# Optimization experiments

Measured on AMD Instinct MI355X. Metric: run time of the kernel, lower is better.

## Reference

```python
import jax, jax.numpy as jnp
import numpy as np

B, T, F = 1024, 256, 124
H = 64
ADIM = 4


def setup_inputs() -> dict:
    key = jax.random.key(0)
    ks = jax.random.split(key, 8)
    s = 0.05
    return {
        "x": jax.random.normal(ks[0], (B, T, F), dtype=jnp.float32),
        "previous_actions": jax.random.normal(ks[1], (B, T, ADIM), dtype=jnp.float32),
        "Wx": jax.random.normal(ks[2], (F + ADIM, 4 * H), dtype=jnp.float32) * s,
        "Wh": jax.random.normal(ks[3], (H, 4 * H), dtype=jnp.float32) * s,
        "b": jnp.zeros((4 * H,), dtype=jnp.float32),
        "W1": jax.random.normal(ks[4], (T * H, 64), dtype=jnp.float32) * s,
        "b1": jnp.zeros((64,), dtype=jnp.float32),
        "W2": jax.random.normal(ks[5], (64, 64), dtype=jnp.float32) * s,
        "b2": jnp.zeros((64,), dtype=jnp.float32),
        "W3": jax.random.normal(ks[6], (64, 2 * ADIM), dtype=jnp.float32) * s,
        "b3": jnp.zeros((2 * ADIM,), dtype=jnp.float32),
    }


def _lstm_scan(xs, Wx, Wh, b):
    # xs: [B, T, D]; returns final (c, h) and all hidden states [B, T, H]
    bsz = xs.shape[0]
    h_dim = Wh.shape[0]
    # precompute input projections once (big GEMM), scan only does h @ Wh
    xproj = jnp.einsum('btd,dg->btg', xs, Wx) + b  # [B, T, 4H]

    def step(carry, xp):
        c, h = carry
        gates = xp + h @ Wh  # [B, 4H]
        i, f, g, o = jnp.split(gates, 4, axis=-1)
        i = jax.nn.sigmoid(i)
        f = jax.nn.sigmoid(f)
        g = jnp.tanh(g)
        o = jax.nn.sigmoid(o)
        c = f * c + i * g
        h = o * jnp.tanh(c)
        return (c, h), h

    c0 = jnp.zeros((bsz, h_dim), xs.dtype)
    h0 = jnp.zeros((bsz, h_dim), xs.dtype)
    (c, h), hs = jax.lax.scan(step, (c0, h0), jnp.swapaxes(xproj, 0, 1))
    return (c, h), jnp.swapaxes(hs, 0, 1)  # hs: [B, T, H]


def reference(x, previous_actions, Wx, Wh, b, W1, b1, W2, b2, W3, b3):
    bsz, seq = x.shape[0], x.shape[1]
    xf = x.reshape((bsz, seq, -1))
    xs = jnp.concatenate([xf, previous_actions], axis=-1)  # [B, T, F+4]
    (c, h), hs = _lstm_scan(xs, Wx, Wh, b)
    flat = hs.reshape((bsz, -1))  # [B, T*H] -- module flattens ALL timesteps
    a = jax.nn.relu(flat @ W1 + b1)
    a = jax.nn.relu(a @ W2 + b2)
    actor = a @ W3 + b3  # [B, 2*action_dim]
    return actor, (c, h)
```

## Files before the change

kernel.cpp:

```cpp
#include <hip/hip_runtime.h>
#include <hip/hip_bf16.h>
#include <stdint.h>

static constexpr int Bsz = 1024;
static constexpr int TT  = 256;
static constexpr int FF  = 124;
static constexpr int HH  = 64;
static constexpr int GG  = 256;
static constexpr int BB  = 16;
static constexpr int C_OFF = Bsz * 8;
static constexpr int H_OFF = C_OFF + Bsz * HH;

static constexpr int WXH_U16 = 24 * 256 * 8;
static constexpr int W1P_U16 = 256 * 4096;
static constexpr size_t WS_NEED = (size_t)(WXH_U16 + W1P_U16) * 2;

static constexpr int XS0 = 0;
static constexpr int XP0 = 65536;
static constexpr int HB0 = 131072;
static constexpr int MA0 = 135168;
static constexpr int MB0 = 139328;
static constexpr int POOLSZ = 143488;

typedef __attribute__((ext_vector_type(8))) short bf16x8;
typedef __attribute__((ext_vector_type(4))) float f32x4;

#define MFMA16 __builtin_amdgcn_mfma_f32_16x16x32_bf16

__device__ __forceinline__ uint16_t f2bf(float x) {
  union { float f; uint32_t u; } v; v.f = x;
  return (uint16_t)((v.u + 0x7FFFu + ((v.u >> 16) & 1u)) >> 16);
}
__device__ __forceinline__ uint32_t cvtpk(float lo, float hi) {
  uint32_t r;
  asm("v_cvt_pk_bf16_f32 %0, %1, %2" : "=v"(r) : "v"(lo), "v"(hi));
  return r;
}
__device__ __forceinline__ uint16_t bf1(float x) { return (uint16_t)cvtpk(x, x); }
__device__ __forceinline__ float fsig(float x) {
  return __builtin_amdgcn_rcpf(1.0f + __builtin_amdgcn_exp2f(-1.4426950408889634f * x));
}
__device__ __forceinline__ float ftanh(float x) {
  float e = __builtin_amdgcn_exp2f(-2.8853900817779268f * x);
  return (1.0f - e) * __builtin_amdgcn_rcpf(1.0f + e);
}
__device__ __forceinline__ bf16x8 cvt8(float4 a, float4 b) {
  union { uint32_t u[4]; bf16x8 v; } r;
  r.u[0] = cvtpk(a.x, a.y); r.u[1] = cvtpk(a.z, a.w);
  r.u[2] = cvtpk(b.x, b.y); r.u[3] = cvtpk(b.z, b.w);
  return r.v;
}
__device__ __forceinline__ void dma16(const void* g, void* l) {
  __builtin_amdgcn_global_load_lds(
      (const __attribute__((address_space(1))) uint32_t*)g,
      (__attribute__((address_space(3))) uint32_t*)l, 16, 0, 0);
}

__global__ __launch_bounds__(256) void pack_weights(
    const float* __restrict__ Wx, const float* __restrict__ Wh,
    const float* __restrict__ W1, uint16_t* __restrict__ wsp)
{
  const int c = blockIdx.x * 256 + threadIdx.x;
  uint16_t v[8];
  size_t dst;
  if (c < 6144) {
    const int f = c >> 8, tid = c & 255;
    const int w = tid >> 6, l = tid & 63;
    const int kgl = (l >> 4) * 8, r16 = l & 15;
    if (f < 16) {
      const int g = f >> 2, kf = f & 3;
      const int col = g * 64 + w * 16 + r16;
#pragma unroll
      for (int j = 0; j < 8; ++j) v[j] = f2bf(Wx[(size_t)(kf * 32 + kgl + j) * GG + col]);
    } else {
      const int g = (f - 16) >> 1, kf = (f - 16) & 1;
      const int col = g * 64 + w * 16 + r16;
#pragma unroll
      for (int j = 0; j < 8; ++j) v[j] = f2bf(Wh[(size_t)(kf * 32 + kgl + j) * GG + col]);
    }
    dst = (size_t)c * 8;
  } else if (c < 6144 + 131072) {
    const int cc = c - 6144;
    const int t = cc >> 9, r = cc & 511;
    const int w = r >> 7, half = (r >> 6) & 1, l = r & 63;
    const int row0 = t * 64 + half * 32 + (l >> 4) * 8;
    const int col = w * 16 + (l & 15);
#pragma unroll
    for (int j = 0; j < 8; ++j) v[j] = f2bf(W1[(size_t)(row0 + j) * 64 + col]);
    dst = (size_t)WXH_U16 + (size_t)cc * 8;
  } else return;
  uint4 pk;
  pk.x = (uint32_t)v[0] | ((uint32_t)v[1] << 16);
  pk.y = (uint32_t)v[2] | ((uint32_t)v[3] << 16);
  pk.z = (uint32_t)v[4] | ((uint32_t)v[5] << 16);
  pk.w = (uint32_t)v[6] | ((uint32_t)v[7] << 16);
  *(uint4*)(wsp + dst) = pk;
}


#define PER_PROD(PRT, U) { \
  asm volatile("s_waitcnt vmcnt(6)" ::: "memory"); \
  const bool live_ = (PRT) + 2 < TT; \
  bf16x8 ax0, ax1, ax2, ax3; \
  if (live_) { \
    const char* xb = pool + (((U) + 2) & 7) * 8192; \
    float4 y0 = *(const float4*)(xb + offx0); \
    float4 y1 = *(const float4*)(xb + offx1); \
    float4 y2 = *(const float4*)(xb + offx2); \
    float4 y3 = *(const float4*)(xb + offx3); \
    ax0 = cvt8(y0, y1); ax1 = cvt8(y2, y3); \
    float4 y4 = *(const float4*)(xb + offx4); \
    float4 y5 = *(const float4*)(xb + offx5); \
    float4 y6 = *(const float4*)(xb + offx6); \
    float4 y7 = *(const float4*)(xb + offx7); \
    ax2 = cvt8(y4, y5); ax3 = cvt8(y6, y7); \
  } \
  { char* ld = pool + (((U) + 6) & 7) * 8192 + pw * 2048; \
    dma16(gsrc0, ld); dma16(gsrc1, ld + 1024); } \
  if ((PRT) + 7 < TT) { gsrc0 += inc0; gsrc1 += inc1; } \
  if (live_) { \
    char* xpw = pool + XP0 + (((U) + 2) & 3) * 16384 + pw * 4096 + l * 16; \
    _Pragma("unroll") \
    for (int g = 0; g < 4; ++g) { \
      f32x4 acc = {bias4[g], bias4[g], bias4[g], bias4[g]}; \
      acc = MFMA16(ax0, bwx[g][0], acc, 0, 0, 0); \
      acc = MFMA16(ax1, bwx[g][1], acc, 0, 0, 0); \
      acc = MFMA16(ax2, bwx[g][2], acc, 0, 0, 0); \
      acc = MFMA16(ax3, bwx[g][3], acc, 0, 0, 0); \
      *(f32x4*)(xpw + g * 1024) = acc; \
    } \
  } }

#define PER_CONS(PRT, U) { \
  const uint16_t* w1p = wsp + (size_t)WXH_U16 + ((size_t)(PRT) * 512 + cs * 128 + l) * 8; \
  bf16x8 nw1a = *(const bf16x8*)(w1p); \
  bf16x8 nw1b = *(const bf16x8*)(w1p + 512); \
  const char* xpb = pool + XP0 + ((U) & 3) * 16384 + cs * 4096 + l * 16; \
  f32x4 a0 = *(const f32x4*)(xpb); \
  f32x4 a1 = *(const f32x4*)(xpb + 1024); \
  f32x4 a2 = *(const f32x4*)(xpb + 2048); \
  f32x4 a3 = *(const f32x4*)(xpb + 3072); \
  const char* hb = pool + HB0 + ((U) & 1) * 2048; \
  bf16x8 ah0 = *(const bf16x8*)(hb + row16 * 128 + (((0 + kg) << 4) ^ swz)); \
  bf16x8 ah1 = *(const bf16x8*)(hb + row16 * 128 + (((4 + kg) << 4) ^ swz)); \
  a0 = MFMA16(ah0, bwh[0][0], a0, 0, 0, 0); \
  a1 = MFMA16(ah0, bwh[1][0], a1, 0, 0, 0); \
  a2 = MFMA16(ah0, bwh[2][0], a2, 0, 0, 0); \
  a3 = MFMA16(ah0, bwh[3][0], a3, 0, 0, 0); \
  a0 = MFMA16(ah1, bwh[0][1], a0, 0, 0, 0); \
  a1 = MFMA16(ah1, bwh[1][1], a1, 0, 0, 0); \
  a2 = MFMA16(ah1, bwh[2][1], a2, 0, 0, 0); \
  a3 = MFMA16(ah1, bwh[3][1], a3, 0, 0, 0); \
  wacc = MFMA16(ah0, cw1a, wacc, 0, 0, 0); \
  wacc = MFMA16(ah1, cw1b, wacc, 0, 0, 0); \
  cw1a = nw1a; cw1b = nw1b; \
  char* hw = pool + HB0 + (((U) & 1) ^ 1) * 2048; \
  _Pragma("unroll") \
  for (int jj = 0; jj < 4; ++jj) { \
    float i_ = fsig(a0[jj]); \
    float f_ = fsig(a1[jj]); \
    float gv = ftanh(a2[jj]); \
    float o_ = fsig(a3[jj]); \
    float cn = f_ * cacc[jj] + i_ * gv; \
    cacc[jj] = cn; \
    float hv = o_ * ftanh(cn); \
    const int row = kg * 4 + jj; \
    *(uint16_t*)(hw + row * 128 + (((kcol >> 3) << 4) ^ ((row & 7) << 4)) + (kcol & 7) * 2) = bf1(hv); \
  } }

#define PERIOD(PRT, U) { \
  if (w < 4) { PER_CONS(PRT, U) } else { PER_PROD(PRT, U) } \
  asm volatile("s_waitcnt lgkmcnt(0)\n\ts_barrier" ::: "memory"); }

__global__ __launch_bounds__(512, 2)
void actor_pc(
    const float* __restrict__ x,  const float* __restrict__ pa,
    const float* __restrict__ bg, const uint16_t* __restrict__ wsp,
    const float* __restrict__ b1, const float* __restrict__ W2,
    const float* __restrict__ b2, const float* __restrict__ W3,
    const float* __restrict__ b3, float* __restrict__ out)
{
  __shared__ __align__(16) char pool[POOLSZ];

  const int tid   = threadIdx.x;
  const int w     = tid >> 6;
  const int cs    = w & 3;
  const int pw    = w & 3;
  const int l     = tid & 63;
  const int row16 = l & 15;
  const int kg    = l >> 4;
  const int b0    = blockIdx.x * BB;
  const int swz   = (row16 & 7) << 4;
  const int kcol  = cs * 16 + row16;

  if (w < 4) __builtin_amdgcn_s_setprio(1);

  bf16x8 bwx[4][4];
  bf16x8 bwh[4][2];
  float  bias4[4];
  bf16x8 cw1a = {}, cw1b = {};
  float  cacc[4] = {0.f, 0.f, 0.f, 0.f};
  f32x4  wacc = {0.f, 0.f, 0.f, 0.f};

  int offx0, offx1, offx2, offx3, offx4, offx5, offx6, offx7;
  {
    const int rb = row16 * 512, r7 = row16 & 7;
#define OX(kf, lh) (rb + ((((kf) * 8 + kg * 2 + (lh)) ^ r7) << 4))
    offx0 = OX(0, 0); offx1 = OX(0, 1); offx2 = OX(1, 0); offx3 = OX(1, 1);
    offx4 = OX(2, 0); offx5 = OX(2, 1); offx6 = OX(3, 0); offx7 = OX(3, 1);
#undef OX
  }
  const char* gsrc0; const char* gsrc1; int inc0 = 0, inc1 = 0;
  {
#define GSRC(j, G, INC) { \
    const int d = pw * 2 + (j); \
    const int row = d * 2 + (l >> 5); \
    const int c_swz = l & 31; \
    const int c_or = c_swz ^ (row & 7); \
    const size_t rb_ = (size_t)(b0 + row) * TT; \
    if (c_or == 31) { G = (const char*)(pa + rb_ * 4); INC = 16; } \
    else { G = (const char*)(x + rb_ * FF + c_or * 4); INC = FF * 4; } }
    GSRC(0, gsrc0, inc0)
    GSRC(1, gsrc1, inc1)
#undef GSRC
  }

  if (w >= 4) {
#pragma unroll
    for (int g = 0; g < 4; ++g) {
#pragma unroll
      for (int kf = 0; kf < 4; ++kf)
        bwx[g][kf] = *(const bf16x8*)(wsp + ((size_t)(g * 4 + kf) * 256 + pw * 64 + l) * 8);
      bias4[g] = bg[g * 64 + pw * 16 + row16];
    }
#pragma unroll
    for (int s = 0; s < 6; ++s) {
      char* ld = pool + s * 8192 + pw * 2048;
      dma16(gsrc0, ld); dma16(gsrc1, ld + 1024);
      gsrc0 += inc0; gsrc1 += inc1;
    }
  } else {
#pragma unroll
    for (int g = 0; g < 4; ++g)
#pragma unroll
      for (int kf = 0; kf < 2; ++kf)
        bwh[g][kf] = *(const bf16x8*)(wsp + ((size_t)(16 + g * 2 + kf) * 256 + cs * 64 + l) * 8);
    const uint16_t* w1p = wsp + (size_t)WXH_U16 + ((size_t)cs * 128 + l) * 8;
    cw1a = *(const bf16x8*)(w1p);
    cw1b = *(const bf16x8*)(w1p + 512);
  }
  if (tid < 256) ((uint64_t*)(pool + HB0))[tid] = 0ull;

#define PRE(TSTEP, VMC) \
  if (w >= 4) { \
    asm volatile("s_waitcnt vmcnt(" #VMC ")" ::: "memory"); \
    const char* xb = pool + (TSTEP) * 8192; \
    float4 y0 = *(const float4*)(xb + offx0), y1 = *(const float4*)(xb + offx1); \
    float4 y2 = *(const float4*)(xb + offx2), y3 = *(const float4*)(xb + offx3); \
    float4 y4 = *(const float4*)(xb + offx4), y5 = *(const float4*)(xb + offx5); \
    float4 y6 = *(const float4*)(xb + offx6), y7 = *(const float4*)(xb + offx7); \
    bf16x8 ax0 = cvt8(y0, y1), ax1 = cvt8(y2, y3), ax2 = cvt8(y4, y5), ax3 = cvt8(y6, y7); \
    char* xpw = pool + XP0 + (TSTEP) * 16384 + pw * 4096 + l * 16; \
    _Pragma("unroll") \
    for (int g = 0; g < 4; ++g) { \
      f32x4 acc = {bias4[g], bias4[g], bias4[g], bias4[g]}; \
      acc = MFMA16(ax0, bwx[g][0], acc, 0, 0, 0); \
      acc = MFMA16(ax1, bwx[g][1], acc, 0, 0, 0); \
      acc = MFMA16(ax2, bwx[g][2], acc, 0, 0, 0); \
      acc = MFMA16(ax3, bwx[g][3], acc, 0, 0, 0); \
      *(f32x4*)(xpw + g * 1024) = acc; \
    } \
  } \
  asm volatile("s_waitcnt lgkmcnt(0)\n\ts_barrier" ::: "memory");

  PRE(0, 10)
  PRE(1, 8)
#undef PRE

#pragma unroll 1
  for (int pp = 0; pp < TT; pp += 8) {
    PERIOD(pp + 0, 0) PERIOD(pp + 1, 1) PERIOD(pp + 2, 2) PERIOD(pp + 3, 3)
    PERIOD(pp + 4, 4) PERIOD(pp + 5, 5) PERIOD(pp + 6, 6) PERIOD(pp + 7, 7)
  }

  __syncthreads();

  {
    float* w2l = (float*)pool;
    for (int i = tid; i < 4096; i += 512) w2l[i] = W2[i];
  }

  if (w < 4) {
    const char* hb = pool + HB0;
    bf16x8 at0 = *(const bf16x8*)(hb + row16 * 128 + (((0 + kg) << 4) ^ swz));
    bf16x8 at1 = *(const bf16x8*)(hb + row16 * 128 + (((4 + kg) << 4) ^ swz));
    wacc = MFMA16(at0, cw1a, wacc, 0, 0, 0);
    wacc = MFMA16(at1, cw1b, wacc, 0, 0, 0);
    const float bv = b1[kcol];
    float* mlpa = (float*)(pool + MA0);
#pragma unroll
    for (int jj = 0; jj < 4; ++jj) {
      const int row = kg * 4 + jj;
      mlpa[row * 65 + kcol] = fmaxf(wacc[jj] + bv, 0.f);
      out[C_OFF + (size_t)(b0 + row) * HH + kcol] = cacc[jj];
      uint32_t hu = *(const uint16_t*)(hb + row * 128 +
                    (((kcol >> 3) << 4) ^ ((row & 7) << 4)) + (kcol & 7) * 2);
      union { uint32_t u; float f; } hf_; hf_.u = hu << 16;
      out[H_OFF + (size_t)(b0 + row) * HH + kcol] = hf_.f;
    }
  }
  __syncthreads();
  {
    const float* mlpa = (const float*)(pool + MA0);
    const float* w2l  = (const float*)pool;
    float* mlpb = (float*)(pool + MB0);
    const int b = tid >> 5, j0 = tid & 31;
    float s0 = b2[j0], s1 = b2[j0 + 32];
#pragma unroll 8
    for (int k = 0; k < 64; ++k) {
      const float av = mlpa[b * 65 + k];
      s0 += av * w2l[k * 64 + j0];
      s1 += av * w2l[k * 64 + j0 + 32];
    }
    mlpb[b * 65 + j0]      = fmaxf(s0, 0.f);
    mlpb[b * 65 + j0 + 32] = fmaxf(s1, 0.f);
  }
  __syncthreads();
  if (tid < 128) {
    const float* mlpb = (const float*)(pool + MB0);
    const int b = tid >> 3, jj = tid & 7;
    float s = b3[jj];
#pragma unroll 8
    for (int k = 0; k < 64; ++k) s += mlpb[b * 65 + k] * W3[(size_t)k * 8 + jj];
    out[(size_t)(b0 + b) * 8 + jj] = s;
  }
}

__global__ __launch_bounds__(256, 1) void actor_fused_fb(
    const float* __restrict__ x,  const float* __restrict__ pa,
    const float* __restrict__ Wx, const float* __restrict__ Wh,
    const float* __restrict__ bg, const float* __restrict__ W1,
    const float* __restrict__ b1, const float* __restrict__ W2,
    const float* __restrict__ b2, const float* __restrict__ W3,
    const float* __restrict__ b3, float* __restrict__ out)
{
  __shared__ __align__(16) uint16_t xs_lds[2][BB * 128];
  __shared__ __align__(16) uint16_t h_lds[2][BB * HH];
  __shared__ float w2_lds[64 * 64];
  __shared__ float mlp_a[BB * 65];
  __shared__ float mlp_b[BB * 65];

  const int tid = threadIdx.x, w = tid >> 6, l = tid & 63;
  const int row16 = l & 15, kg = l >> 4;
  const int b0 = blockIdx.x * BB, swz = (row16 & 7) << 4;

  bf16x8 bwx[4][4], bwh[4][2];
  float bias4[4];
#pragma unroll
  for (int g = 0; g < 4; ++g) {
    const int col = g * 64 + w * 16 + row16;
    bias4[g] = bg[col];
#pragma unroll
    for (int kf = 0; kf < 4; ++kf)
#pragma unroll
      for (int j = 0; j < 8; ++j)
        bwx[g][kf][j] = (short)f2bf(Wx[(size_t)(kf * 32 + kg * 8 + j) * GG + col]);
#pragma unroll
    for (int kf = 0; kf < 2; ++kf)
#pragma unroll
      for (int j = 0; j < 8; ++j)
        bwh[g][kf][j] = (short)f2bf(Wh[(size_t)(kf * 32 + kg * 8 + j) * GG + col]);
  }
  for (int i = tid; i < 64 * 64; i += 256) w2_lds[i] = W2[i];
  reinterpret_cast<uint64_t*>(&h_lds[0][0])[tid] = 0ull;

  const int srow = tid >> 4, li = tid & 15;
  const int st_byte = srow * 256 + ((li << 4) ^ ((srow & 7) << 4));
  {
    const size_t base = (size_t)(b0 + srow) * TT + 0;
    float4 fa, fb;
    if (li < 15) { fa = *(const float4*)(x + base * FF + li * 8);
                   fb = *(const float4*)(x + base * FF + li * 8 + 4); }
    else         { fa = *(const float4*)(x + base * FF + 120);
                   fb = *(const float4*)(pa + base * 4); }
    uint4 pk;
    pk.x = (uint32_t)f2bf(fa.x) | ((uint32_t)f2bf(fa.y) << 16);
    pk.y = (uint32_t)f2bf(fa.z) | ((uint32_t)f2bf(fa.w) << 16);
    pk.z = (uint32_t)f2bf(fb.x) | ((uint32_t)f2bf(fb.y) << 16);
    pk.w = (uint32_t)f2bf(fb.z) | ((uint32_t)f2bf(fb.w) << 16);
    *(uint4*)((char*)&xs_lds[0][0] + st_byte) = pk;
  }
  float4 pfa, pfb;
  {
    const size_t base = (size_t)(b0 + srow) * TT + 1;
    if (li < 15) { pfa = *(const float4*)(x + base * FF + li * 8);
                   pfb = *(const float4*)(x + base * FF + li * 8 + 4); }
    else         { pfa = *(const float4*)(x + base * FF + 120);
                   pfb = *(const float4*)(pa + base * 4); }
  }
  __syncthreads();

  f32x4 cacc = {0.f, 0.f, 0.f, 0.f};
  f32x4 wacc = {0.f, 0.f, 0.f, 0.f};
  int cur = 0;

  for (int t = 0; t < TT; ++t) {
    {
      uint4 pk;
      pk.x = (uint32_t)f2bf(pfa.x) | ((uint32_t)f2bf(pfa.y) << 16);
      pk.y = (uint32_t)f2bf(pfa.z) | ((uint32_t)f2bf(pfa.w) << 16);
      pk.z = (uint32_t)f2bf(pfb.x) | ((uint32_t)f2bf(pfb.y) << 16);
      pk.w = (uint32_t)f2bf(pfb.z) | ((uint32_t)f2bf(pfb.w) << 16);
      *(uint4*)((char*)&xs_lds[cur ^ 1][0] + st_byte) = pk;
    }
    {
      const int tp = (t + 2 < TT) ? (t + 2) : (TT - 1);
      const size_t base = (size_t)(b0 + srow) * TT + tp;
      if (li < 15) { pfa = *(const float4*)(x + base * FF + li * 8);
                     pfb = *(const float4*)(x + base * FF + li * 8 + 4); }
      else         { pfa = *(const float4*)(x + base * FF + 120);
                     pfb = *(const float4*)(pa + base * 4); }
    }
    bf16x8 bw1a, bw1b;
    if (t > 0) {
      const size_t r0 = (size_t)(t - 1) * 64 + kg * 8;
      const int c1w = w * 16 + row16;
#pragma unroll
      for (int j = 0; j < 8; ++j) {
        bw1a[j] = (short)f2bf(W1[(r0 + j) * 64 + c1w]);
        bw1b[j] = (short)f2bf(W1[(r0 + 32 + j) * 64 + c1w]);
      }
    }
    const char* xb = (const char*)&xs_lds[cur][0];
    const char* hb = (const char*)&h_lds[cur][0];
    bf16x8 ax0 = *(const bf16x8*)(xb + row16 * 256 + (((0 * 4 + kg) << 4) ^ swz));
    bf16x8 ax1 = *(const bf16x8*)(xb + row16 * 256 + (((1 * 4 + kg) << 4) ^ swz));
    bf16x8 ax2 = *(const bf16x8*)(xb + row16 * 256 + (((2 * 4 + kg) << 4) ^ swz));
    bf16x8 ax3 = *(const bf16x8*)(xb + row16 * 256 + (((3 * 4 + kg) << 4) ^ swz));
    bf16x8 ah0 = *(const bf16x8*)(hb + row16 * 128 + (((0 + kg) << 4) ^ swz));
    bf16x8 ah1 = *(const bf16x8*)(hb + row16 * 128 + (((4 + kg) << 4) ^ swz));

    f32x4 g0 = {bias4[0], bias4[0], bias4[0], bias4[0]};
    f32x4 g1 = {bias4[1], bias4[1], bias4[1], bias4[1]};
    f32x4 g2 = {bias4[2], bias4[2], bias4[2], bias4[2]};
    f32x4 g3 = {bias4[3], bias4[3], bias4[3], bias4[3]};
    g0 = MFMA16(ax0, bwx[0][0], g0, 0, 0, 0);
    g1 = MFMA16(ax0, bwx[1][0], g1, 0, 0, 0);
    g2 = MFMA16(ax0, bwx[2][0], g2, 0, 0, 0);
    g3 = MFMA16(ax0, bwx[3][0], g3, 0, 0, 0);
    g0 = MFMA16(ax1, bwx[0][1], g0, 0, 0, 0);
    g1 = MFMA16(ax1, bwx[1][1], g1, 0, 0, 0);
    g2 = MFMA16(ax1, bwx[2][1], g2, 0, 0, 0);
    g3 = MFMA16(ax1, bwx[3][1], g3, 0, 0, 0);
    g0 = MFMA16(ax2, bwx[0][2], g0, 0, 0, 0);
    g1 = MFMA16(ax2, bwx[1][2], g1, 0, 0, 0);
    g2 = MFMA16(ax2, bwx[2][2], g2, 0, 0, 0);
    g3 = MFMA16(ax2, bwx[3][2], g3, 0, 0, 0);
    g0 = MFMA16(ax3, bwx[0][3], g0, 0, 0, 0);
    g1 = MFMA16(ax3, bwx[1][3], g1, 0, 0, 0);
    g2 = MFMA16(ax3, bwx[2][3], g2, 0, 0, 0);
    g3 = MFMA16(ax3, bwx[3][3], g3, 0, 0, 0);
    g0 = MFMA16(ah0, bwh[0][0], g0, 0, 0, 0);
    g1 = MFMA16(ah0, bwh[1][0], g1, 0, 0, 0);
    g2 = MFMA16(ah0, bwh[2][0], g2, 0, 0, 0);
    g3 = MFMA16(ah0, bwh[3][0], g3, 0, 0, 0);
    g0 = MFMA16(ah1, bwh[0][1], g0, 0, 0, 0);
    g1 = MFMA16(ah1, bwh[1][1], g1, 0, 0, 0);
    g2 = MFMA16(ah1, bwh[2][1], g2, 0, 0, 0);
    g3 = MFMA16(ah1, bwh[3][1], g3, 0, 0, 0);
    if (t > 0) {
      wacc = MFMA16(ah0, bw1a, wacc, 0, 0, 0);
      wacc = MFMA16(ah1, bw1b, wacc, 0, 0, 0);
    }
    const int kcol = w * 16 + row16;
#pragma unroll
    for (int jj = 0; jj < 4; ++jj) {
      float i_ = fsig(g0[jj]);
      float f_ = fsig(g1[jj]);
      float gv = ftanh(g2[jj]);
      float o_ = fsig(g3[jj]);
      float cn = f_ * cacc[jj] + i_ * gv;
      cacc[jj] = cn;
      float hv = o_ * ftanh(cn);
      const int row = kg * 4 + jj;
      *(uint16_t*)((char*)&h_lds[cur ^ 1][0] + row * 128 +
                   (((kcol >> 3) << 4) ^ ((row & 7) << 4)) + (kcol & 7) * 2) = f2bf(hv);
      if (t == TT - 1) {
        out[C_OFF + (size_t)(b0 + row) * HH + kcol] = cn;
        out[H_OFF + (size_t)(b0 + row) * HH + kcol] = hv;
      }
    }
    __syncthreads();
    cur ^= 1;
  }
  {
    const char* hb = (const char*)&h_lds[cur][0];
    bf16x8 at0 = *(const bf16x8*)(hb + row16 * 128 + (((0 + kg) << 4) ^ swz));
    bf16x8 at1 = *(const bf16x8*)(hb + row16 * 128 + (((4 + kg) << 4) ^ swz));
    bf16x8 bw1a, bw1b;
    const size_t r0 = (size_t)(TT - 1) * 64 + kg * 8;
    const int c1w = w * 16 + row16;
#pragma unroll
    for (int j = 0; j < 8; ++j) {
      bw1a[j] = (short)f2bf(W1[(r0 + j) * 64 + c1w]);
      bw1b[j] = (short)f2bf(W1[(r0 + 32 + j) * 64 + c1w]);
    }
    wacc = MFMA16(at0, bw1a, wacc, 0, 0, 0);
    wacc = MFMA16(at1, bw1b, wacc, 0, 0, 0);
  }
  {
    const int kcol = w * 16 + row16;
    const float bv = b1[kcol];
#pragma unroll
    for (int jj = 0; jj < 4; ++jj)
      mlp_a[(kg * 4 + jj) * 65 + kcol] = fmaxf(wacc[jj] + bv, 0.f);
  }
  __syncthreads();
  {
    const int b = tid >> 4, j0 = tid & 15;
    float s0 = b2[j0], s1 = b2[j0 + 16], s2 = b2[j0 + 32], s3 = b2[j0 + 48];
#pragma unroll 8
    for (int k = 0; k < 64; ++k) {
      const float av = mlp_a[b * 65 + k];
      s0 += av * w2_lds[k * 64 + j0];
      s1 += av * w2_lds[k * 64 + j0 + 16];
      s2 += av * w2_lds[k * 64 + j0 + 32];
      s3 += av * w2_lds[k * 64 + j0 + 48];
    }
    mlp_b[b * 65 + j0]      = fmaxf(s0, 0.f);
    mlp_b[b * 65 + j0 + 16] = fmaxf(s1, 0.f);
    mlp_b[b * 65 + j0 + 32] = fmaxf(s2, 0.f);
    mlp_b[b * 65 + j0 + 48] = fmaxf(s3, 0.f);
  }
  __syncthreads();
  if (tid < 128) {
    const int b = tid >> 3, jj = tid & 7;
    float s = b3[jj];
#pragma unroll 8
    for (int k = 0; k < 64; ++k) s += mlp_b[b * 65 + k] * W3[(size_t)k * 8 + jj];
    out[(size_t)(b0 + b) * 8 + jj] = s;
  }
}

extern "C" void kernel_launch(void* const* d_in, const int* in_sizes, int n_in,
                              void* d_out, int out_size, void* d_ws, size_t ws_size,
                              hipStream_t stream) {
  const float* x  = (const float*)d_in[0];
  const float* pa = (const float*)d_in[1];
  const float* Wx = (const float*)d_in[2];
  const float* Wh = (const float*)d_in[3];
  const float* bg = (const float*)d_in[4];
  const float* W1 = (const float*)d_in[5];
  const float* b1 = (const float*)d_in[6];
  const float* W2 = (const float*)d_in[7];
  const float* b2 = (const float*)d_in[8];
  const float* W3 = (const float*)d_in[9];
  const float* b3 = (const float*)d_in[10];
  (void)in_sizes; (void)n_in; (void)out_size;

  if (ws_size >= WS_NEED) {
    uint16_t* wsp = (uint16_t*)d_ws;
    pack_weights<<<dim3(536), dim3(256), 0, stream>>>(Wx, Wh, W1, wsp);
    actor_pc<<<dim3(Bsz / BB), dim3(512), 0, stream>>>(
        x, pa, bg, wsp, b1, W2, b2, W3, b3, (float*)d_out);
  } else {
    actor_fused_fb<<<dim3(Bsz / BB), dim3(256), 0, stream>>>(
        x, pa, Wx, Wh, bg, W1, b1, W2, b2, W3, b3, (float*)d_out);
  }
}
```

Before: 189.3 us.

## Merge producer/consumer warps into single 4-wave block with register-held input projections

Replaces the 8-wave producer/consumer warp-specialized LSTM kernel with a 4-wave kernel where every wave computes the next step's input projection itself and keeps it in registers (double-buffered XPA/XPB), eliminating the LDS round-trip for xproj. W1 tiles are now streamed into an LDS ring via async DMA instead of per-step global loads. This shrinks LDS use and halves threads, trading inter-wave overlap for lower LDS traffic and register pressure on the serial recurrence path.

New measurement: 210.0 us. 1.11x slower.

```diff
diff --git a/kernel.cpp b/kernel.cpp
--- a/kernel.cpp
+++ b/kernel.cpp
@@ -15,12 +15,12 @@
 static constexpr int W1P_U16 = 256 * 4096;
 static constexpr size_t WS_NEED = (size_t)(WXH_U16 + W1P_U16) * 2;
 
-static constexpr int XS0 = 0;
-static constexpr int XP0 = 65536;
-static constexpr int HB0 = 131072;
-static constexpr int MA0 = 135168;
-static constexpr int MB0 = 139328;
-static constexpr int POOLSZ = 143488;
+static constexpr int XS0  = 0;
+static constexpr int W1R0 = 65536;
+static constexpr int HB0  = 98304;
+static constexpr int MA0  = 102400;
+static constexpr int MB0  = 106560;
+static constexpr int POOLSZ = 110720;
 
 typedef __attribute__((ext_vector_type(8))) short bf16x8;
 typedef __attribute__((ext_vector_type(4))) float f32x4;
@@ -97,52 +97,15 @@
   *(uint4*)(wsp + dst) = pk;
 }
 
-
-#define PER_PROD(PRT, U) { \
-  asm volatile("s_waitcnt vmcnt(6)" ::: "memory"); \
-  const bool live_ = (PRT) + 2 < TT; \
-  bf16x8 ax0, ax1, ax2, ax3; \
-  if (live_) { \
-    const char* xb = pool + (((U) + 2) & 7) * 8192; \
-    float4 y0 = *(const float4*)(xb + offx0); \
-    float4 y1 = *(const float4*)(xb + offx1); \
-    float4 y2 = *(const float4*)(xb + offx2); \
-    float4 y3 = *(const float4*)(xb + offx3); \
-    ax0 = cvt8(y0, y1); ax1 = cvt8(y2, y3); \
-    float4 y4 = *(const float4*)(xb + offx4); \
-    float4 y5 = *(const float4*)(xb + offx5); \
-    float4 y6 = *(const float4*)(xb + offx6); \
-    float4 y7 = *(const float4*)(xb + offx7); \
-    ax2 = cvt8(y4, y5); ax3 = cvt8(y6, y7); \
-  } \
-  { char* ld = pool + (((U) + 6) & 7) * 8192 + pw * 2048; \
-    dma16(gsrc0, ld); dma16(gsrc1, ld + 1024); } \
-  if ((PRT) + 7 < TT) { gsrc0 += inc0; gsrc1 += inc1; } \
-  if (live_) { \
-    char* xpw = pool + XP0 + (((U) + 2) & 3) * 16384 + pw * 4096 + l * 16; \
-    _Pragma("unroll") \
-    for (int g = 0; g < 4; ++g) { \
-      f32x4 acc = {bias4[g], bias4[g], bias4[g], bias4[g]}; \
-      acc = MFMA16(ax0, bwx[g][0], acc, 0, 0, 0); \
-      acc = MFMA16(ax1, bwx[g][1], acc, 0, 0, 0); \
-      acc = MFMA16(ax2, bwx[g][2], acc, 0, 0, 0); \
-      acc = MFMA16(ax3, bwx[g][3], acc, 0, 0, 0); \
-      *(f32x4*)(xpw + g * 1024) = acc; \
-    } \
-  } }
-
-#define PER_CONS(PRT, U) { \
-  const uint16_t* w1p = wsp + (size_t)WXH_U16 + ((size_t)(PRT) * 512 + cs * 128 + l) * 8; \
-  bf16x8 nw1a = *(const bf16x8*)(w1p); \
-  bf16x8 nw1b = *(const bf16x8*)(w1p + 512); \
-  const char* xpb = pool + XP0 + ((U) & 3) * 16384 + cs * 4096 + l * 16; \
-  f32x4 a0 = *(const f32x4*)(xpb); \
-  f32x4 a1 = *(const f32x4*)(xpb + 1024); \
-  f32x4 a2 = *(const f32x4*)(xpb + 2048); \
-  f32x4 a3 = *(const f32x4*)(xpb + 3072); \
-  const char* hb = pool + HB0 + ((U) & 1) * 2048; \
+#define PERIOD(PRT, XPU, XPN) { \
+  asm volatile("s_waitcnt vmcnt(4)" ::: "memory"); \
+  const char* hb = pool + HB0 + ((PRT) & 1) * 2048; \
   bf16x8 ah0 = *(const bf16x8*)(hb + row16 * 128 + (((0 + kg) << 4) ^ swz)); \
   bf16x8 ah1 = *(const bf16x8*)(hb + row16 * 128 + (((4 + kg) << 4) ^ swz)); \
+  const char* wbp = pool + W1R0 + (((PRT) + 3) & 3) * 8192 + w * 2048 + l * 16; \
+  bf16x8 bw1a = *(const bf16x8*)(wbp); \
+  bf16x8 bw1b = *(const bf16x8*)(wbp + 1024); \
+  f32x4 a0 = XPU[0], a1 = XPU[1], a2 = XPU[2], a3 = XPU[3]; \
   a0 = MFMA16(ah0, bwh[0][0], a0, 0, 0, 0); \
   a1 = MFMA16(ah0, bwh[1][0], a1, 0, 0, 0); \
   a2 = MFMA16(ah0, bwh[2][0], a2, 0, 0, 0); \
@@ -151,10 +114,38 @@
   a1 = MFMA16(ah1, bwh[1][1], a1, 0, 0, 0); \
   a2 = MFMA16(ah1, bwh[2][1], a2, 0, 0, 0); \
   a3 = MFMA16(ah1, bwh[3][1], a3, 0, 0, 0); \
-  wacc = MFMA16(ah0, cw1a, wacc, 0, 0, 0); \
-  wacc = MFMA16(ah1, cw1b, wacc, 0, 0, 0); \
-  cw1a = nw1a; cw1b = nw1b; \
-  char* hw = pool + HB0 + (((U) & 1) ^ 1) * 2048; \
+  wacc = MFMA16(ah0, bw1a, wacc, 0, 0, 0); \
+  wacc = MFMA16(ah1, bw1b, wacc, 0, 0, 0); \
+  if ((PRT) + 1 < TT) { \
+    const char* xb = pool + (((PRT) + 1) & 7) * 8192; \
+    float4 y0 = *(const float4*)(xb + offx0); \
+    float4 y1 = *(const float4*)(xb + offx1); \
+    float4 y2 = *(const float4*)(xb + offx2); \
+    float4 y3 = *(const float4*)(xb + offx3); \
+    float4 y4 = *(const float4*)(xb + offx4); \
+    float4 y5 = *(const float4*)(xb + offx5); \
+    float4 y6 = *(const float4*)(xb + offx6); \
+    float4 y7 = *(const float4*)(xb + offx7); \
+    bf16x8 ax0 = cvt8(y0, y1), ax1 = cvt8(y2, y3); \
+    bf16x8 ax2 = cvt8(y4, y5), ax3 = cvt8(y6, y7); \
+    _Pragma("unroll") \
+    for (int g = 0; g < 4; ++g) { \
+      f32x4 accg = {bias4[g], bias4[g], bias4[g], bias4[g]}; \
+      accg = MFMA16(ax0, bwx[g][0], accg, 0, 0, 0); \
+      accg = MFMA16(ax1, bwx[g][1], accg, 0, 0, 0); \
+      accg = MFMA16(ax2, bwx[g][2], accg, 0, 0, 0); \
+      accg = MFMA16(ax3, bwx[g][3], accg, 0, 0, 0); \
+      XPN[g] = accg; \
+    } \
+  } \
+  { const int wb_ = ((PRT) + 2 < TT) ? (PRT) + 2 : TT - 1; \
+    const char* gs = w1g + (size_t)wb_ * 8192 + w * 2048 + l * 16; \
+    char* ld = pool + W1R0 + (((PRT) + 2) & 3) * 8192 + w * 2048; \
+    dma16(gs, ld); dma16(gs + 1024, ld + 1024); } \
+  { char* ld = pool + (((PRT) + 4) & 7) * 8192 + w * 2048; \
+    dma16(gsrc0, ld); dma16(gsrc1, ld + 1024); \
+    if ((PRT) + 5 < TT) { gsrc0 += inc0; gsrc1 += inc1; } } \
+  char* hw = pool + HB0 + (((PRT) & 1) ^ 1) * 2048; \
   _Pragma("unroll") \
   for (int jj = 0; jj < 4; ++jj) { \
     float i_ = fsig(a0[jj]); \
@@ -166,14 +157,11 @@
     float hv = o_ * ftanh(cn); \
     const int row = kg * 4 + jj; \
     *(uint16_t*)(hw + row * 128 + (((kcol >> 3) << 4) ^ ((row & 7) << 4)) + (kcol & 7) * 2) = bf1(hv); \
-  } }
-
-#define PERIOD(PRT, U) { \
-  if (w < 4) { PER_CONS(PRT, U) } else { PER_PROD(PRT, U) } \
+  } \
   asm volatile("s_waitcnt lgkmcnt(0)\n\ts_barrier" ::: "memory"); }
 
-__global__ __launch_bounds__(512, 2)
-void actor_pc(
+__global__ __launch_bounds__(256, 1)
+void actor_merged(
     const float* __restrict__ x,  const float* __restrict__ pa,
     const float* __restrict__ bg, const uint16_t* __restrict__ wsp,
     const float* __restrict__ b1, const float* __restrict__ W2,
@@ -184,23 +172,20 @@
 
   const int tid   = threadIdx.x;
   const int w     = tid >> 6;
-  const int cs    = w & 3;
-  const int pw    = w & 3;
   const int l     = tid & 63;
   const int row16 = l & 15;
   const int kg    = l >> 4;
   const int b0    = blockIdx.x * BB;
   const int swz   = (row16 & 7) << 4;
-  const int kcol  = cs * 16 + row16;
-
-  if (w < 4) __builtin_amdgcn_s_setprio(1);
+  const int kcol  = w * 16 + row16;
+  const char* w1g = (const char*)(wsp + WXH_U16);
 
   bf16x8 bwx[4][4];
   bf16x8 bwh[4][2];
   float  bias4[4];
-  bf16x8 cw1a = {}, cw1b = {};
   float  cacc[4] = {0.f, 0.f, 0.f, 0.f};
   f32x4  wacc = {0.f, 0.f, 0.f, 0.f};
+  f32x4  XPA[4], XPB[4];
 
   int offx0, offx1, offx2, offx3, offx4, offx5, offx6, offx7;
   {
@@ -213,7 +198,7 @@
   const char* gsrc0; const char* gsrc1; int inc0 = 0, inc1 = 0;
   {
 #define GSRC(j, G, INC) { \
-    const int d = pw * 2 + (j); \
+    const int d = w * 2 + (j); \
     const int row = d * 2 + (l >> 5); \
     const int c_swz = l & 31; \
     const int c_or = c_swz ^ (row & 7); \
@@ -225,77 +210,73 @@
 #undef GSRC
   }
 
-  if (w >= 4) {
+#pragma unroll
+  for (int g = 0; g < 4; ++g) {
+#pragma unroll
+    for (int kf = 0; kf < 4; ++kf)
+      bwx[g][kf] = *(const bf16x8*)(wsp + ((size_t)(g * 4 + kf) * 256 + w * 64 + l) * 8);
+#pragma unroll
+    for (int kf = 0; kf < 2; ++kf)
+      bwh[g][kf] = *(const bf16x8*)(wsp + ((size_t)(16 + g * 2 + kf) * 256 + w * 64 + l) * 8);
+    bias4[g] = bg[g * 64 + w * 16 + row16];
+  }
+  ((uint64_t*)(pool + HB0))[tid] = 0ull;
+
+  {
+    const char* gsW = w1g + w * 2048 + l * 16;
+    { char* ld = pool + W1R0 + 3 * 8192 + w * 2048; dma16(gsW, ld); dma16(gsW + 1024, ld + 1024); }
+    { char* ld = pool + 0 * 8192 + w * 2048; dma16(gsrc0, ld); dma16(gsrc1, ld + 1024); gsrc0 += inc0; gsrc1 += inc1; }
+    { char* ld = pool + 1 * 8192 + w * 2048; dma16(gsrc0, ld); dma16(gsrc1, ld + 1024); gsrc0 += inc0; gsrc1 += inc1; }
+    { char* ld = pool + W1R0 + 0 * 8192 + w * 2048; dma16(gsW, ld); dma16(gsW + 1024, ld + 1024); }
+    { char* ld = pool + 2 * 8192 + w * 2048; dma16(gsrc0, ld); dma16(gsrc1, ld + 1024); gsrc0 += inc0; gsrc1 += inc1; }
+    { const char* gs1 = w1g + 8192 + w * 2048 + l * 16;
+      char* ld = pool + W1R0 + 1 * 8192 + w * 2048; dma16(gs1, ld); dma16(gs1 + 1024, ld + 1024); }
+    { char* ld = pool + 3 * 8192 + w * 2048; dma16(gsrc0, ld); dma16(gsrc1, ld + 1024); gsrc0 += inc0; gsrc1 += inc1; }
+  }
+  asm volatile("s_waitcnt vmcnt(8) lgkmcnt(0)\n\ts_barrier" ::: "memory");
+
+  {
+    const char* xb = pool + 0 * 8192;
+    float4 y0 = *(const float4*)(xb + offx0), y1 = *(const float4*)(xb + offx1);
+    float4 y2 = *(const float4*)(xb + offx2), y3 = *(const float4*)(xb + offx3);
+    float4 y4 = *(const float4*)(xb + offx4), y5 = *(const float4*)(xb + offx5);
+    float4 y6 = *(const float4*)(xb + offx6), y7 = *(const float4*)(xb + offx7);
+    bf16x8 ax0 = cvt8(y0, y1), ax1 = cvt8(y2, y3), ax2 = cvt8(y4, y5), ax3 = cvt8(y6, y7);
 #pragma unroll
     for (int g = 0; g < 4; ++g) {
-#pragma unroll
-      for (int kf = 0; kf < 4; ++kf)
-        bwx[g][kf] = *(const bf16x8*)(wsp + ((size_t)(g * 4 + kf) * 256 + pw * 64 + l) * 8);
-      bias4[g] = bg[g * 64 + pw * 16 + row16];
-    }
-#pragma unroll
-    for (int s = 0; s < 6; ++s) {
-      char* ld = pool + s * 8192 + pw * 2048;
-      dma16(gsrc0, ld); dma16(gsrc1, ld + 1024);
-      gsrc0 += inc0; gsrc1 += inc1;
-    }
-  } else {
-#pragma unroll
-    for (int g = 0; g < 4; ++g)
-#pragma unroll
-      for (int kf = 0; kf < 2; ++kf)
-        bwh[g][kf] = *(const bf16x8*)(wsp + ((size_t)(16 + g * 2 + kf) * 256 + cs * 64 + l) * 8);
-    const uint16_t* w1p = wsp + (size_t)WXH_U16 + ((size_t)cs * 128 + l) * 8;
-    cw1a = *(const bf16x8*)(w1p);
-    cw1b = *(const bf16x8*)(w1p + 512);
-  }
-  if (tid < 256) ((uint64_t*)(pool + HB0))[tid] = 0ull;
-
-#define PRE(TSTEP, VMC) \
-  if (w >= 4) { \
-    asm volatile("s_waitcnt vmcnt(" #VMC ")" ::: "memory"); \
-    const char* xb = pool + (TSTEP) * 8192; \
-    float4 y0 = *(const float4*)(xb + offx0), y1 = *(const float4*)(xb + offx1); \
-    float4 y2 = *(const float4*)(xb + offx2), y3 = *(const float4*)(xb + offx3); \
-    float4 y4 = *(const float4*)(xb + offx4), y5 = *(const float4*)(xb + offx5); \
-    float4 y6 = *(const float4*)(xb + offx6), y7 = *(const float4*)(xb + offx7); \
-    bf16x8 ax0 = cvt8(y0, y1), ax1 = cvt8(y2, y3), ax2 = cvt8(y4, y5), ax3 = cvt8(y6, y7); \
-    char* xpw = pool + XP0 + (TSTEP) * 16384 + pw * 4096 + l * 16; \
-    _Pragma("unroll") \
-    for (int g = 0; g < 4; ++g) { \
-      f32x4 acc = {bias4[g], bias4[g], bias4[g], bias4[g]}; \
-      acc = MFMA16(ax0, bwx[g][0], acc, 0, 0, 0); \
-      acc = MFMA16(ax1, bwx[g][1], acc, 0, 0, 0); \
-      acc = MFMA16(ax2, bwx[g][2], acc, 0, 0, 0); \
-      acc = MFMA16(ax3, bwx[g][3], acc, 0, 0, 0); \
-      *(f32x4*)(xpw + g * 1024) = acc; \
-    } \
-  } \
-  asm volatile("s_waitcnt lgkmcnt(0)\n\ts_barrier" ::: "memory");
-
-  PRE(0, 10)
-  PRE(1, 8)
-#undef PRE
+      f32x4 accg = {bias4[g], bias4[g], bias4[g], bias4[g]};
+      accg = MFMA16(ax0, bwx[g][0], accg, 0, 0, 0);
+      accg = MFMA16(ax1, bwx[g][1], accg, 0, 0, 0);
+      accg = MFMA16(ax2, bwx[g][2], accg, 0, 0, 0);
+      accg = MFMA16(ax3, bwx[g][3], accg, 0, 0, 0);
+      XPA[g] = accg;
+    }
+  }
 
 #pragma unroll 1
   for (int pp = 0; pp < TT; pp += 8) {
-    PERIOD(pp + 0, 0) PERIOD(pp + 1, 1) PERIOD(pp + 2, 2) PERIOD(pp + 3, 3)
-    PERIOD(pp + 4, 4) PERIOD(pp + 5, 5) PERIOD(pp + 6, 6) PERIOD(pp + 7, 7)
+    PERIOD(pp + 0, XPA, XPB) PERIOD(pp + 1, XPB, XPA)
+    PERIOD(pp + 2, XPA, XPB) PERIOD(pp + 3, XPB, XPA)
+    PERIOD(pp + 4, XPA, XPB) PERIOD(pp + 5, XPB, XPA)
+    PERIOD(pp + 6, XPA, XPB) PERIOD(pp + 7, XPB, XPA)
   }
 
   __syncthreads();
 
   {
     float* w2l = (float*)pool;
-    for (int i = tid; i < 4096; i += 512) w2l[i] = W2[i];
-  }
-
-  if (w < 4) {
+    for (int i = tid; i < 4096; i += 256) w2l[i] = W2[i];
+  }
+
+  {
     const char* hb = pool + HB0;
     bf16x8 at0 = *(const bf16x8*)(hb + row16 * 128 + (((0 + kg) << 4) ^ swz));
     bf16x8 at1 = *(const bf16x8*)(hb + row16 * 128 + (((4 + kg) << 4) ^ swz));
-    wacc = MFMA16(at0, cw1a, wacc, 0, 0, 0);
-    wacc = MFMA16(at1, cw1b, wacc, 0, 0, 0);
+    const char* wbp = pool + W1R0 + 3 * 8192 + w * 2048 + l * 16;
+    bf16x8 ba = *(const bf16x8*)(wbp);
+    bf16x8 bb = *(const bf16x8*)(wbp + 1024);
+    wacc = MFMA16(at0, ba, wacc, 0, 0, 0);
+    wacc = MFMA16(at1, bb, wacc, 0, 0, 0);
     const float bv = b1[kcol];
     float* mlpa = (float*)(pool + MA0);
 #pragma unroll
@@ -305,8 +286,8 @@
       out[C_OFF + (size_t)(b0 + row) * HH + kcol] = cacc[jj];
       uint32_t hu = *(const uint16_t*)(hb + row * 128 +
                     (((kcol >> 3) << 4) ^ ((row & 7) << 4)) + (kcol & 7) * 2);
-      union { uint32_t u; float f; } hf_; hf_.u = hu << 16;
-      out[H_OFF + (size_t)(b0 + row) * HH + kcol] = hf_.f;
+      union { uint32_t u; float f; } cv_; cv_.u = hu << 16;
+      out[H_OFF + (size_t)(b0 + row) * HH + kcol] = cv_.f;
     }
   }
   __syncthreads();
@@ -314,16 +295,20 @@
     const float* mlpa = (const float*)(pool + MA0);
     const float* w2l  = (const float*)pool;
     float* mlpb = (float*)(pool + MB0);
-    const int b = tid >> 5, j0 = tid & 31;
-    float s0 = b2[j0], s1 = b2[j0 + 32];
+    const int b = tid >> 4, j0 = tid & 15;
+    float s0 = b2[j0], s1 = b2[j0 + 16], s2 = b2[j0 + 32], s3 = b2[j0 + 48];
 #pragma unroll 8
     for (int k = 0; k < 64; ++k) {
       const float av = mlpa[b * 65 + k];
       s0 += av * w2l[k * 64 + j0];
-      s1 += av * w2l[k * 64 + j0 + 32];
+      s1 += av * w2l[k * 64 + j0 + 16];
+      s2 += av * w2l[k * 64 + j0 + 32];
+      s3 += av * w2l[k * 64 + j0 + 48];
     }
     mlpb[b * 65 + j0]      = fmaxf(s0, 0.f);
-    mlpb[b * 65 + j0 + 32] = fmaxf(s1, 0.f);
+    mlpb[b * 65 + j0 + 16] = fmaxf(s1, 0.f);
+    mlpb[b * 65 + j0 + 32] = fmaxf(s2, 0.f);
+    mlpb[b * 65 + j0 + 48] = fmaxf(s3, 0.f);
   }
   __syncthreads();
   if (tid < 128) {
@@ -561,7 +546,7 @@
   if (ws_size >= WS_NEED) {
     uint16_t* wsp = (uint16_t*)d_ws;
     pack_weights<<<dim3(536), dim3(256), 0, stream>>>(Wx, Wh, W1, wsp);
-    actor_pc<<<dim3(Bsz / BB), dim3(512), 0, stream>>>(
+    actor_merged<<<dim3(Bsz / BB), dim3(256), 0, stream>>>(
         x, pa, bg, wsp, b1, W2, b2, W3, b3, (float*)d_out);
   } else {
     actor_fused_fb<<<dim3(Bsz / BB), dim3(256), 0, stream>>>(
```

## Move input projection MFMAs into consumer waves, producers only convert x to bf16

Applied to the files above, without the earlier changes.

The kernel previously had producer waves compute the full x@Wx projection and stage fp32 gate pre-activations in LDS. Now producers only convert each x tile to bf16 and write it to a small swizzled LDS buffer, and consumer waves do the x@Wx MFMAs together with h@Wh on the recurrent critical path. This cuts LDS use (the pool shrinks from about 143 KB to 94 KB) and LDS traffic. The cost is four times more MFMAs on the serial recurrence path in the consumer waves, plus extra weight registers held there.

After: 182.1 us. 1.04x faster.

```diff
diff --git a/kernel.cpp b/kernel.cpp
--- a/kernel.cpp
+++ b/kernel.cpp
@@ -16,11 +16,11 @@
 static constexpr size_t WS_NEED = (size_t)(WXH_U16 + W1P_U16) * 2;
 
 static constexpr int XS0 = 0;
-static constexpr int XP0 = 65536;
-static constexpr int HB0 = 131072;
-static constexpr int MA0 = 135168;
-static constexpr int MB0 = 139328;
-static constexpr int POOLSZ = 143488;
+static constexpr int BX0 = 65536;
+static constexpr int HB0 = 81920;
+static constexpr int MA0 = 86016;
+static constexpr int MB0 = 90176;
+static constexpr int POOLSZ = 94336;
 
 typedef __attribute__((ext_vector_type(8))) short bf16x8;
 typedef __attribute__((ext_vector_type(4))) float f32x4;
@@ -98,69 +98,70 @@
 }
 
 
-#define PER_PROD(PRT, U) { \
+#define PER_CVT(PRT, U) { \
   asm volatile("s_waitcnt vmcnt(6)" ::: "memory"); \
-  const bool live_ = (PRT) + 2 < TT; \
-  bf16x8 ax0, ax1, ax2, ax3; \
-  if (live_) { \
+  if ((PRT) + 2 < TT) { \
     const char* xb = pool + (((U) + 2) & 7) * 8192; \
-    float4 y0 = *(const float4*)(xb + offx0); \
-    float4 y1 = *(const float4*)(xb + offx1); \
-    float4 y2 = *(const float4*)(xb + offx2); \
-    float4 y3 = *(const float4*)(xb + offx3); \
-    ax0 = cvt8(y0, y1); ax1 = cvt8(y2, y3); \
-    float4 y4 = *(const float4*)(xb + offx4); \
-    float4 y5 = *(const float4*)(xb + offx5); \
-    float4 y6 = *(const float4*)(xb + offx6); \
-    float4 y7 = *(const float4*)(xb + offx7); \
-    ax2 = cvt8(y4, y5); ax3 = cvt8(y6, y7); \
+    float4 ya = *(const float4*)(xb + offxA); \
+    float4 yb = *(const float4*)(xb + offxB); \
+    bf16x8 bv = cvt8(ya, yb); \
+    *(bf16x8*)(pool + BX0 + (((U) + 2) & 3) * 4096 + row16 * 256 + \
+               (((pw * 4 + kg) << 4) ^ swz)) = bv; \
   } \
   { char* ld = pool + (((U) + 6) & 7) * 8192 + pw * 2048; \
     dma16(gsrc0, ld); dma16(gsrc1, ld + 1024); } \
-  if ((PRT) + 7 < TT) { gsrc0 += inc0; gsrc1 += inc1; } \
-  if (live_) { \
-    char* xpw = pool + XP0 + (((U) + 2) & 3) * 16384 + pw * 4096 + l * 16; \
-    _Pragma("unroll") \
-    for (int g = 0; g < 4; ++g) { \
-      f32x4 acc = {bias4[g], bias4[g], bias4[g], bias4[g]}; \
-      acc = MFMA16(ax0, bwx[g][0], acc, 0, 0, 0); \
-      acc = MFMA16(ax1, bwx[g][1], acc, 0, 0, 0); \
-      acc = MFMA16(ax2, bwx[g][2], acc, 0, 0, 0); \
-      acc = MFMA16(ax3, bwx[g][3], acc, 0, 0, 0); \
-      *(f32x4*)(xpw + g * 1024) = acc; \
-    } \
-  } }
+  if ((PRT) + 7 < TT) { gsrc0 += inc0; gsrc1 += inc1; } }
 
 #define PER_CONS(PRT, U) { \
   const uint16_t* w1p = wsp + (size_t)WXH_U16 + ((size_t)(PRT) * 512 + cs * 128 + l) * 8; \
   bf16x8 nw1a = *(const bf16x8*)(w1p); \
   bf16x8 nw1b = *(const bf16x8*)(w1p + 512); \
-  const char* xpb = pool + XP0 + ((U) & 3) * 16384 + cs * 4096 + l * 16; \
-  f32x4 a0 = *(const f32x4*)(xpb); \
-  f32x4 a1 = *(const f32x4*)(xpb + 1024); \
-  f32x4 a2 = *(const f32x4*)(xpb + 2048); \
-  f32x4 a3 = *(const f32x4*)(xpb + 3072); \
+  const char* bx = pool + BX0 + ((U) & 3) * 4096; \
+  bf16x8 ax0 = *(const bf16x8*)(bx + row16 * 256 + (((0 * 4 + kg) << 4) ^ swz)); \
+  bf16x8 ax1 = *(const bf16x8*)(bx + row16 * 256 + (((1 * 4 + kg) << 4) ^ swz)); \
+  bf16x8 ax2 = *(const bf16x8*)(bx + row16 * 256 + (((2 * 4 + kg) << 4) ^ swz)); \
+  bf16x8 ax3 = *(const bf16x8*)(bx + row16 * 256 + (((3 * 4 + kg) << 4) ^ swz)); \
   const char* hb = pool + HB0 + ((U) & 1) * 2048; \
   bf16x8 ah0 = *(const bf16x8*)(hb + row16 * 128 + (((0 + kg) << 4) ^ swz)); \
   bf16x8 ah1 = *(const bf16x8*)(hb + row16 * 128 + (((4 + kg) << 4) ^ swz)); \
-  a0 = MFMA16(ah0, bwh[0][0], a0, 0, 0, 0); \
-  a1 = MFMA16(ah0, bwh[1][0], a1, 0, 0, 0); \
-  a2 = MFMA16(ah0, bwh[2][0], a2, 0, 0, 0); \
-  a3 = MFMA16(ah0, bwh[3][0], a3, 0, 0, 0); \
-  a0 = MFMA16(ah1, bwh[0][1], a0, 0, 0, 0); \
-  a1 = MFMA16(ah1, bwh[1][1], a1, 0, 0, 0); \
-  a2 = MFMA16(ah1, bwh[2][1], a2, 0, 0, 0); \
-  a3 = MFMA16(ah1, bwh[3][1], a3, 0, 0, 0); \
+  f32x4 g0 = {bias4[0], bias4[0], bias4[0], bias4[0]}; \
+  f32x4 g1 = {bias4[1], bias4[1], bias4[1], bias4[1]}; \
+  f32x4 g2 = {bias4[2], bias4[2], bias4[2], bias4[2]}; \
+  f32x4 g3 = {bias4[3], bias4[3], bias4[3], bias4[3]}; \
+  g0 = MFMA16(ax0, bwx[0][0], g0, 0, 0, 0); \
+  g1 = MFMA16(ax0, bwx[1][0], g1, 0, 0, 0); \
+  g2 = MFMA16(ax0, bwx[2][0], g2, 0, 0, 0); \
+  g3 = MFMA16(ax0, bwx[3][0], g3, 0, 0, 0); \
+  g0 = MFMA16(ax1, bwx[0][1], g0, 0, 0, 0); \
+  g1 = MFMA16(ax1, bwx[1][1], g1, 0, 0, 0); \
+  g2 = MFMA16(ax1, bwx[2][1], g2, 0, 0, 0); \
+  g3 = MFMA16(ax1, bwx[3][1], g3, 0, 0, 0); \
+  g0 = MFMA16(ax2, bwx[0][2], g0, 0, 0, 0); \
+  g1 = MFMA16(ax2, bwx[1][2], g1, 0, 0, 0); \
+  g2 = MFMA16(ax2, bwx[2][2], g2, 0, 0, 0); \
+  g3 = MFMA16(ax2, bwx[3][2], g3, 0, 0, 0); \
+  g0 = MFMA16(ax3, bwx[0][3], g0, 0, 0, 0); \
+  g1 = MFMA16(ax3, bwx[1][3], g1, 0, 0, 0); \
+  g2 = MFMA16(ax3, bwx[2][3], g2, 0, 0, 0); \
+  g3 = MFMA16(ax3, bwx[3][3], g3, 0, 0, 0); \
+  g0 = MFMA16(ah0, bwh[0][0], g0, 0, 0, 0); \
+  g1 = MFMA16(ah0, bwh[1][0], g1, 0, 0, 0); \
+  g2 = MFMA16(ah0, bwh[2][0], g2, 0, 0, 0); \
+  g3 = MFMA16(ah0, bwh[3][0], g3, 0, 0, 0); \
+  g0 = MFMA16(ah1, bwh[0][1], g0, 0, 0, 0); \
+  g1 = MFMA16(ah1, bwh[1][1], g1, 0, 0, 0); \
+  g2 = MFMA16(ah1, bwh[2][1], g2, 0, 0, 0); \
+  g3 = MFMA16(ah1, bwh[3][1], g3, 0, 0, 0); \
   wacc = MFMA16(ah0, cw1a, wacc, 0, 0, 0); \
   wacc = MFMA16(ah1, cw1b, wacc, 0, 0, 0); \
   cw1a = nw1a; cw1b = nw1b; \
   char* hw = pool + HB0 + (((U) & 1) ^ 1) * 2048; \
   _Pragma("unroll") \
   for (int jj = 0; jj < 4; ++jj) { \
-    float i_ = fsig(a0[jj]); \
-    float f_ = fsig(a1[jj]); \
-    float gv = ftanh(a2[jj]); \
-    float o_ = fsig(a3[jj]); \
+    float i_ = fsig(g0[jj]); \
+    float f_ = fsig(g1[jj]); \
+    float gv = ftanh(g2[jj]); \
+    float o_ = fsig(g3[jj]); \
     float cn = f_ * cacc[jj] + i_ * gv; \
     cacc[jj] = cn; \
     float hv = o_ * ftanh(cn); \
@@ -169,11 +170,11 @@
   } }
 
 #define PERIOD(PRT, U) { \
-  if (w < 4) { PER_CONS(PRT, U) } else { PER_PROD(PRT, U) } \
+  if (w < 4) { PER_CONS(PRT, U) } else { PER_CVT(PRT, U) } \
   asm volatile("s_waitcnt lgkmcnt(0)\n\ts_barrier" ::: "memory"); }
 
 __global__ __launch_bounds__(512, 2)
-void actor_pc(
+void actor_sx(
     const float* __restrict__ x,  const float* __restrict__ pa,
     const float* __restrict__ bg, const uint16_t* __restrict__ wsp,
     const float* __restrict__ b1, const float* __restrict__ W2,
@@ -202,13 +203,11 @@
   float  cacc[4] = {0.f, 0.f, 0.f, 0.f};
   f32x4  wacc = {0.f, 0.f, 0.f, 0.f};
 
-  int offx0, offx1, offx2, offx3, offx4, offx5, offx6, offx7;
+  int offxA, offxB;
   {
     const int rb = row16 * 512, r7 = row16 & 7;
-#define OX(kf, lh) (rb + ((((kf) * 8 + kg * 2 + (lh)) ^ r7) << 4))
-    offx0 = OX(0, 0); offx1 = OX(0, 1); offx2 = OX(1, 0); offx3 = OX(1, 1);
-    offx4 = OX(2, 0); offx5 = OX(2, 1); offx6 = OX(3, 0); offx7 = OX(3, 1);
-#undef OX
+    offxA = rb + (((pw * 8 + kg * 2 + 0) ^ r7) << 4);
+    offxB = rb + (((pw * 8 + kg * 2 + 1) ^ r7) << 4);
   }
   const char* gsrc0; const char* gsrc1; int inc0 = 0, inc1 = 0;
   {
@@ -227,13 +226,6 @@
 
   if (w >= 4) {
 #pragma unroll
-    for (int g = 0; g < 4; ++g) {
-#pragma unroll
-      for (int kf = 0; kf < 4; ++kf)
-        bwx[g][kf] = *(const bf16x8*)(wsp + ((size_t)(g * 4 + kf) * 256 + pw * 64 + l) * 8);
-      bias4[g] = bg[g * 64 + pw * 16 + row16];
-    }
-#pragma unroll
     for (int s = 0; s < 6; ++s) {
       char* ld = pool + s * 8192 + pw * 2048;
       dma16(gsrc0, ld); dma16(gsrc1, ld + 1024);
@@ -241,10 +233,15 @@
     }
   } else {
 #pragma unroll
-    for (int g = 0; g < 4; ++g)
+    for (int g = 0; g < 4; ++g) {
+#pragma unroll
+      for (int kf = 0; kf < 4; ++kf)
+        bwx[g][kf] = *(const bf16x8*)(wsp + ((size_t)(g * 4 + kf) * 256 + cs * 64 + l) * 8);
 #pragma unroll
       for (int kf = 0; kf < 2; ++kf)
         bwh[g][kf] = *(const bf16x8*)(wsp + ((size_t)(16 + g * 2 + kf) * 256 + cs * 64 + l) * 8);
+      bias4[g] = bg[g * 64 + cs * 16 + row16];
+    }
     const uint16_t* w1p = wsp + (size_t)WXH_U16 + ((size_t)cs * 128 + l) * 8;
     cw1a = *(const bf16x8*)(w1p);
     cw1b = *(const bf16x8*)(w1p + 512);
@@ -255,21 +252,11 @@
   if (w >= 4) { \
     asm volatile("s_waitcnt vmcnt(" #VMC ")" ::: "memory"); \
     const char* xb = pool + (TSTEP) * 8192; \
-    float4 y0 = *(const float4*)(xb + offx0), y1 = *(const float4*)(xb + offx1); \
-    float4 y2 = *(const float4*)(xb + offx2), y3 = *(const float4*)(xb + offx3); \
-    float4 y4 = *(const float4*)(xb + offx4), y5 = *(const float4*)(xb + offx5); \
-    float4 y6 = *(const float4*)(xb + offx6), y7 = *(const float4*)(xb + offx7); \
-    bf16x8 ax0 = cvt8(y0, y1), ax1 = cvt8(y2, y3), ax2 = cvt8(y4, y5), ax3 = cvt8(y6, y7); \
-    char* xpw = pool + XP0 + (TSTEP) * 16384 + pw * 4096 + l * 16; \
-    _Pragma("unroll") \
-    for (int g = 0; g < 4; ++g) { \
-      f32x4 acc = {bias4[g], bias4[g], bias4[g], bias4[g]}; \
-      acc = MFMA16(ax0, bwx[g][0], acc, 0, 0, 0); \
-      acc = MFMA16(ax1, bwx[g][1], acc, 0, 0, 0); \
-      acc = MFMA16(ax2, bwx[g][2], acc, 0, 0, 0); \
-      acc = MFMA16(ax3, bwx[g][3], acc, 0, 0, 0); \
-      *(f32x4*)(xpw + g * 1024) = acc; \
-    } \
+    float4 ya = *(const float4*)(xb + offxA); \
+    float4 yb = *(const float4*)(xb + offxB); \
+    bf16x8 bv = cvt8(ya, yb); \
+    *(bf16x8*)(pool + BX0 + (TSTEP) * 4096 + row16 * 256 + \
+               (((pw * 4 + kg) << 4) ^ swz)) = bv; \
   } \
   asm volatile("s_waitcnt lgkmcnt(0)\n\ts_barrier" ::: "memory");
 
@@ -305,8 +292,8 @@
       out[C_OFF + (size_t)(b0 + row) * HH + kcol] = cacc[jj];
       uint32_t hu = *(const uint16_t*)(hb + row * 128 +
                     (((kcol >> 3) << 4) ^ ((row & 7) << 4)) + (kcol & 7) * 2);
-      union { uint32_t u; float f; } hf_; hf_.u = hu << 16;
-      out[H_OFF + (size_t)(b0 + row) * HH + kcol] = hf_.f;
+      union { uint32_t u; float f; } cv_; cv_.u = hu << 16;
+      out[H_OFF + (size_t)(b0 + row) * HH + kcol] = cv_.f;
     }
   }
   __syncthreads();
@@ -561,7 +548,7 @@
   if (ws_size >= WS_NEED) {
     uint16_t* wsp = (uint16_t*)d_ws;
     pack_weights<<<dim3(536), dim3(256), 0, stream>>>(Wx, Wh, W1, wsp);
-    actor_pc<<<dim3(Bsz / BB), dim3(512), 0, stream>>>(
+    actor_sx<<<dim3(Bsz / BB), dim3(512), 0, stream>>>(
         x, pa, bg, wsp, b1, W2, b2, W3, b3, (float*)d_out);
   } else {
     actor_fused_fb<<<dim3(Bsz / BB), dim3(256), 0, stream>>>(
```
